# Kernel tuning notes

Measured on AMD Instinct MI355X. Metric: run time of the kernel, lower is better.

Reference implementation:

```python
import jax, jax.numpy as jnp
import numpy as np

N_NODES = 100000
EMB = 16
HID = 64
N_EDGES = 4194304


def setup_inputs() -> dict:
    key = jax.random.key(0)
    k_emb, k_e, k1, k2, k3 = jax.random.split(key, 5)
    node_embeddings = jax.random.normal(k_emb, (N_NODES, EMB), dtype=jnp.float32)
    edge_index = jax.random.randint(k_e, (2, N_EDGES), 0, N_NODES, dtype=jnp.int32)
    # MLP params: Linear(2*EMB -> HID), Linear(HID -> HID//2), Linear(HID//2 -> 1)
    s1 = 1.0 / np.sqrt(2 * EMB)
    s2 = 1.0 / np.sqrt(HID)
    s3 = 1.0 / np.sqrt(HID // 2)
    W1 = jax.random.uniform(k1, (2 * EMB, HID), jnp.float32, -s1, s1)
    b1 = jnp.zeros((HID,), jnp.float32)
    W2 = jax.random.uniform(k2, (HID, HID // 2), jnp.float32, -s2, s2)
    b2 = jnp.zeros((HID // 2,), jnp.float32)
    W3 = jax.random.uniform(k3, (HID // 2, 1), jnp.float32, -s3, s3)
    b3 = jnp.zeros((1,), jnp.float32)
    return {"node_embeddings": node_embeddings, "edge_index": edge_index,
            "W1": W1, "b1": b1, "W2": W2, "b2": b2, "W3": W3, "b3": b3}


def reference(node_embeddings, edge_index, W1, b1, W2, b2, W3, b3):
    # Gather node-pair embeddings and concat: [E, 2*EMB]
    feats = jnp.concatenate([node_embeddings[edge_index[0]],
                             node_embeddings[edge_index[1]]], axis=1)
    # 3-layer MLP (dropout is identity in eval mode)
    h = jax.nn.relu(feats @ W1 + b1)
    h = jax.nn.relu(h @ W2 + b2)
    edge_probs = jax.nn.sigmoid(h @ W3 + b3)  # [E, 1]
    return edge_probs, edge_index
```

## Files before the change

### kernel.cpp

```cpp
#include <hip/hip_runtime.h>
#include <hip/hip_bf16.h>

#define NEMB 16

typedef short s16x8 __attribute__((ext_vector_type(8)));
typedef float f32x16 __attribute__((ext_vector_type(16)));

__device__ __forceinline__ unsigned int pack_bf16x2_rnd(float lo, float hi) {
    unsigned int ul = __float_as_uint(lo);
    unsigned int uh = __float_as_uint(hi);
    return ((ul + 0x8000u) >> 16) | ((uh + 0x8000u) & 0xffff0000u);
}
__device__ __forceinline__ unsigned int pack_bf16x2_trunc(float lo, float hi) {
    return __builtin_amdgcn_perm(__float_as_uint(hi), __float_as_uint(lo),
                                 0x07060302u);
}

__global__ __launch_bounds__(256) void emb_to_bf16_kernel(
        const float* __restrict__ emb, unsigned int* __restrict__ embT,
        int nWords) {
    int i = (blockIdx.x * 256 + threadIdx.x) * 4;
    if (i + 4 <= nWords) {
        float4 a = *reinterpret_cast<const float4*>(emb + 2 * i);
        float4 b = *reinterpret_cast<const float4*>(emb + 2 * i + 4);
        uint4 r;
        r.x = pack_bf16x2_rnd(a.x, a.y);
        r.y = pack_bf16x2_rnd(a.z, a.w);
        r.z = pack_bf16x2_rnd(b.x, b.y);
        r.w = pack_bf16x2_rnd(b.z, b.w);
        *reinterpret_cast<uint4*>(embT + i) = r;
    } else {
        for (; i < nWords; ++i)
            embT[i] = pack_bf16x2_rnd(emb[2 * i], emb[2 * i + 1]);
    }
}

#define WAVES 4
#define ITERS 8
#define EDGES_PER_BLOCK (WAVES * 32 * ITERS)

__global__ __launch_bounds__(256) void edge_fused3_kernel(
        const unsigned short* __restrict__ embT,
        const int* __restrict__ ei,
        const float* __restrict__ W1, const float* __restrict__ b1,
        const float* __restrict__ W2, const float* __restrict__ b2,
        const float* __restrict__ W3, const float* __restrict__ b3,
        float* __restrict__ out, int nE) {
    const int tid = threadIdx.x;
    const int w  = tid >> 6;
    const int l  = tid & 63;
    const int el = l & 31;
    const int hi = l >> 5;

    s16x8 A1[2][2];
#pragma unroll
    for (int jt = 0; jt < 2; ++jt)
#pragma unroll
        for (int kh = 0; kh < 2; ++kh) {
            s16x8 a;
#pragma unroll
            for (int i = 0; i < 8; ++i) {
                float v = W1[(kh * 16 + hi * 8 + i) * 64 + jt * 32 + el];
                a[i] = (short)((__float_as_uint(v) + 0x8000u) >> 16);
            }
            A1[jt][kh] = a;
        }
    s16x8 A2[4];
#pragma unroll
    for (int f = 0; f < 4; ++f) {
        s16x8 a;
#pragma unroll
        for (int i = 0; i < 8; ++i) {
            float v = W2[(f * 16 + hi * 8 + i) * 32 + el];
            a[i] = (short)((__float_as_uint(v) + 0x8000u) >> 16);
        }
        A2[f] = a;
    }
    f32x16 b1v0, b1v1, b2v;
    float w3v[16];
#pragma unroll
    for (int r = 0; r < 16; ++r) {
        int n = (r & 3) + 8 * (r >> 2) + 4 * hi;
        b1v0[r] = b1[n];
        b1v1[r] = b1[32 + n];
        b2v[r]  = b2[n];
        w3v[r]  = W3[n];
    }
    const float b3v = b3[0];

    const int base0 = blockIdx.x * EDGES_PER_BLOCK + w * 32;

    int sv[ITERS], dv[ITERS];
#pragma unroll
    for (int i = 0; i < ITERS; ++i) {
        int e  = base0 + i * (WAVES * 32) + el;
        int ec = e < nE ? e : (nE - 1);
        sv[i] = ei[ec];
        dv[i] = ei[nE + ec];
    }

    auto GATHER = [&](int s, int d, uint4& es, uint4& ed) {
        es = *reinterpret_cast<const uint4*>(embT + ((size_t)s << 4) + (hi << 3));
        ed = *reinterpret_cast<const uint4*>(embT + ((size_t)d << 4) + (hi << 3));
    };

    auto COMPUTE = [&](uint4 esq, uint4 edq, int it, int s, int d) {
        union { uint4 q; s16x8 v; } es, edr;
        es.q = esq; edr.q = edq;

        f32x16 a0 = __builtin_amdgcn_mfma_f32_32x32x16_bf16(A1[0][0], es.v,  b1v0, 0, 0, 0);
        a0        = __builtin_amdgcn_mfma_f32_32x32x16_bf16(A1[0][1], edr.v, a0,   0, 0, 0);
        f32x16 a1 = __builtin_amdgcn_mfma_f32_32x32x16_bf16(A1[1][0], es.v,  b1v1, 0, 0, 0);
        a1        = __builtin_amdgcn_mfma_f32_32x32x16_bf16(A1[1][1], edr.v, a1,   0, 0, 0);

        union { unsigned int u[4]; s16x8 v; } bf0, bf1, bf2, bf3;
        {
#define MAKE_FRAG(BF, AT, M)                                                   \
            {                                                                  \
                unsigned int x0 = pack_bf16x2_trunc(fmaxf((AT)[8*(M)+0], 0.f), \
                                                    fmaxf((AT)[8*(M)+1], 0.f));\
                unsigned int x1 = pack_bf16x2_trunc(fmaxf((AT)[8*(M)+2], 0.f), \
                                                    fmaxf((AT)[8*(M)+3], 0.f));\
                unsigned int y0 = pack_bf16x2_trunc(fmaxf((AT)[8*(M)+4], 0.f), \
                                                    fmaxf((AT)[8*(M)+5], 0.f));\
                unsigned int y1 = pack_bf16x2_trunc(fmaxf((AT)[8*(M)+6], 0.f), \
                                                    fmaxf((AT)[8*(M)+7], 0.f));\
                asm("v_permlane32_swap_b32 %0, %1" : "+v"(x0), "+v"(y0));      \
                asm("v_permlane32_swap_b32 %0, %1" : "+v"(x1), "+v"(y1));      \
                BF.u[0] = x0; BF.u[1] = x1; BF.u[2] = y0; BF.u[3] = y1;        \
            }
            MAKE_FRAG(bf0, a0, 0)
            MAKE_FRAG(bf1, a0, 1)
            MAKE_FRAG(bf2, a1, 0)
            MAKE_FRAG(bf3, a1, 1)
#undef MAKE_FRAG
        }

        f32x16 acc;
        acc = __builtin_amdgcn_mfma_f32_32x32x16_bf16(A2[0], bf0.v, b2v, 0, 0, 0);
        acc = __builtin_amdgcn_mfma_f32_32x32x16_bf16(A2[1], bf1.v, acc, 0, 0, 0);
        acc = __builtin_amdgcn_mfma_f32_32x32x16_bf16(A2[2], bf2.v, acc, 0, 0, 0);
        acc = __builtin_amdgcn_mfma_f32_32x32x16_bf16(A2[3], bf3.v, acc, 0, 0, 0);

        float pr[16];
#pragma unroll
        for (int r = 0; r < 16; ++r)
            pr[r] = fmaxf(acc[r], 0.0f) * w3v[r];
        float s8[8];
#pragma unroll
        for (int r = 0; r < 8; ++r) s8[r] = pr[2 * r] + pr[2 * r + 1];
        float s4[4];
#pragma unroll
        for (int r = 0; r < 4; ++r) s4[r] = s8[2 * r] + s8[2 * r + 1];
        float v = (s4[0] + s4[1]) + (s4[2] + s4[3]);

        {
            float va = v, vb = v;
            asm("v_permlane32_swap_b32 %0, %1" : "+v"(vb), "+v"(va));
            v = va + vb;
        }

        float p = 1.0f / (1.0f + __expf(-(v + b3v)));

        int e = base0 + it * (WAVES * 32) + el;
        if (e < nE) {
            if (hi == 0) {
                out[e] = p;
                out[nE + e] = (float)s;
            } else {
                out[(size_t)2 * nE + e] = (float)d;
            }
        }
    };

    uint4 esA, edA, esB, edB;
    GATHER(sv[0], dv[0], esA, edA);
#pragma unroll
    for (int it = 0; it < ITERS; it += 2) {
        if (it + 1 < ITERS) GATHER(sv[it + 1], dv[it + 1], esB, edB);
        COMPUTE(esA, edA, it, sv[it], dv[it]);
        if (it + 2 < ITERS) GATHER(sv[it + 2], dv[it + 2], esA, edA);
        if (it + 1 < ITERS) COMPUTE(esB, edB, it + 1, sv[it + 1], dv[it + 1]);
    }
}

__global__ __launch_bounds__(256) void edge_mlp_naive_kernel(
        const float* __restrict__ emb, const int* __restrict__ ei,
        const float* __restrict__ W1, const float* __restrict__ b1,
        const float* __restrict__ W2, const float* __restrict__ b2,
        const float* __restrict__ W3, const float* __restrict__ b3,
        float* __restrict__ out, int nE) {
    __shared__ __align__(16) float sW1[32 * 64];
    __shared__ __align__(16) float sW2[64 * 32];
    __shared__ float sW3[32];
    __shared__ float sB1[64];
    __shared__ float sB2[32];
    __shared__ float sB3;
    for (int i = threadIdx.x; i < 2048; i += 256) {
        sW1[i] = W1[i];
        sW2[i] = W2[i];
    }
    if (threadIdx.x < 64) sB1[threadIdx.x] = b1[threadIdx.x];
    if (threadIdx.x < 32) {
        sW3[threadIdx.x] = W3[threadIdx.x];
        sB2[threadIdx.x] = b2[threadIdx.x];
    }
    if (threadIdx.x == 0) sB3 = b3[0];
    __syncthreads();

    int e = blockIdx.x * 256 + threadIdx.x;
    if (e >= nE) return;

    int s = ei[e];
    int d = ei[nE + e];

    float f[32];
    const float4* ps = reinterpret_cast<const float4*>(emb + (size_t)s * NEMB);
    const float4* pd = reinterpret_cast<const float4*>(emb + (size_t)d * NEMB);
#pragma unroll
    for (int q = 0; q < 4; ++q) {
        float4 v = ps[q];
        f[4 * q + 0] = v.x; f[4 * q + 1] = v.y; f[4 * q + 2] = v.z; f[4 * q + 3] = v.w;
    }
#pragma unroll
    for (int q = 0; q < 4; ++q) {
        float4 v = pd[q];
        f[16 + 4 * q + 0] = v.x; f[16 + 4 * q + 1] = v.y;
        f[16 + 4 * q + 2] = v.z; f[16 + 4 * q + 3] = v.w;
    }

    float h1[64];
#pragma unroll
    for (int j = 0; j < 64; j += 4) {
        float a0 = sB1[j + 0], a1 = sB1[j + 1], a2 = sB1[j + 2], a3 = sB1[j + 3];
#pragma unroll
        for (int k = 0; k < 32; ++k) {
            float4 wv = *reinterpret_cast<const float4*>(sW1 + k * 64 + j);
            a0 = fmaf(f[k], wv.x, a0);
            a1 = fmaf(f[k], wv.y, a1);
            a2 = fmaf(f[k], wv.z, a2);
            a3 = fmaf(f[k], wv.w, a3);
        }
        h1[j + 0] = fmaxf(a0, 0.0f);
        h1[j + 1] = fmaxf(a1, 0.0f);
        h1[j + 2] = fmaxf(a2, 0.0f);
        h1[j + 3] = fmaxf(a3, 0.0f);
    }

    float acc = sB3;
#pragma unroll
    for (int j = 0; j < 32; j += 4) {
        float a0 = sB2[j + 0], a1 = sB2[j + 1], a2 = sB2[j + 2], a3 = sB2[j + 3];
#pragma unroll
        for (int k = 0; k < 64; ++k) {
            float4 wv = *reinterpret_cast<const float4*>(sW2 + k * 32 + j);
            a0 = fmaf(h1[k], wv.x, a0);
            a1 = fmaf(h1[k], wv.y, a1);
            a2 = fmaf(h1[k], wv.z, a2);
            a3 = fmaf(h1[k], wv.w, a3);
        }
        acc = fmaf(fmaxf(a0, 0.0f), sW3[j + 0], acc);
        acc = fmaf(fmaxf(a1, 0.0f), sW3[j + 1], acc);
        acc = fmaf(fmaxf(a2, 0.0f), sW3[j + 2], acc);
        acc = fmaf(fmaxf(a3, 0.0f), sW3[j + 3], acc);
    }

    out[e] = 1.0f / (1.0f + __expf(-acc));
}

__global__ __launch_bounds__(256) void edge_idx_copy_kernel(
        const int* __restrict__ ei, float* __restrict__ out, int n) {
    int i = (blockIdx.x * 256 + threadIdx.x) * 4;
    if (i + 4 <= n) {
        int4 a = *reinterpret_cast<const int4*>(ei + i);
        float4 r = make_float4((float)a.x, (float)a.y, (float)a.z, (float)a.w);
        *reinterpret_cast<float4*>(out + i) = r;
    } else {
        for (; i < n; ++i) out[i] = (float)ei[i];
    }
}

extern "C" void kernel_launch(void* const* d_in, const int* in_sizes, int n_in,
                              void* d_out, int out_size, void* d_ws, size_t ws_size,
                              hipStream_t stream) {
    const float* emb = (const float*)d_in[0];
    const int*   ei  = (const int*)d_in[1];
    const float* W1  = (const float*)d_in[2];
    const float* b1  = (const float*)d_in[3];
    const float* W2  = (const float*)d_in[4];
    const float* b2  = (const float*)d_in[5];
    const float* W3  = (const float*)d_in[6];
    const float* b3  = (const float*)d_in[7];

    const int nNodes = in_sizes[0] / NEMB;
    const int n2E    = in_sizes[1];
    const int nE     = n2E / 2;

    float* out = (float*)d_out;

    const size_t tbl_bytes = (size_t)nNodes * NEMB * sizeof(unsigned short);
    const bool use_ws = (ws_size >= tbl_bytes);

    if (use_ws) {
        unsigned int* embT = (unsigned int*)d_ws;
        const int nWords = nNodes * 8;
        emb_to_bf16_kernel<<<(nWords / 4 + 255) / 256, 256, 0, stream>>>(
            emb, embT, nWords);

        edge_fused3_kernel<<<(nE + EDGES_PER_BLOCK - 1) / EDGES_PER_BLOCK, 256, 0,
                             stream>>>(
            (const unsigned short*)embT, ei, W1, b1, W2, b2, W3, b3, out, nE);
    } else {
        edge_mlp_naive_kernel<<<(nE + 255) / 256, 256, 0, stream>>>(
            emb, ei, W1, b1, W2, b2, W3, b3, out, nE);
        edge_idx_copy_kernel<<<((n2E + 3) / 4 + 255) / 256, 256, 0, stream>>>(
            ei, out + nE, n2E);
    }
}
```

Measured before the change: 87.15 us.

## Split edge MLP into unguarded persistent-loop kernel plus guarded tail kernel

Each block now processes 32 tiles instead of 8 in a rolled software-pipelined loop. Edge indices and embedding gathers are prefetched one to two tiles ahead, and there are no bounds checks. The per-block weight fragment setup is amortized over four times as many edges, and the grid shrinks accordingly. Any remainder edges go to a separate guarded kernel. Costs are fewer blocks in flight to hide gather latency, and an extra kernel launch when a tail exists (none for the test size).

Result: slower. 95.90 us (+10.0%).

```diff
diff --git a/kernel.cpp b/kernel.cpp
--- a/kernel.cpp
+++ b/kernel.cpp
@@ -36,10 +36,114 @@
 }
 
 #define WAVES 4
-#define ITERS 8
-#define EDGES_PER_BLOCK (WAVES * 32 * ITERS)
-
-__global__ __launch_bounds__(256) void edge_fused3_kernel(
+#define ITERS_FLAT 32
+#define EPB_FLAT (WAVES * 32 * ITERS_FLAT)
+#define ITERS_G 8
+#define EPB_G (WAVES * 32 * ITERS_G)
+
+struct MlpConsts {
+    s16x8 A1[2][2];
+    s16x8 A2[4];
+    f32x16 b1v0, b1v1, b2v;
+    float w3v[16];
+    float b3v;
+};
+
+__device__ __forceinline__ void load_consts(
+        MlpConsts& C, int el, int hi,
+        const float* __restrict__ W1, const float* __restrict__ b1,
+        const float* __restrict__ W2, const float* __restrict__ b2,
+        const float* __restrict__ W3, const float* __restrict__ b3) {
+#pragma unroll
+    for (int jt = 0; jt < 2; ++jt)
+#pragma unroll
+        for (int kh = 0; kh < 2; ++kh) {
+            s16x8 a;
+#pragma unroll
+            for (int i = 0; i < 8; ++i) {
+                float v = W1[(kh * 16 + hi * 8 + i) * 64 + jt * 32 + el];
+                a[i] = (short)((__float_as_uint(v) + 0x8000u) >> 16);
+            }
+            C.A1[jt][kh] = a;
+        }
+#pragma unroll
+    for (int f = 0; f < 4; ++f) {
+        s16x8 a;
+#pragma unroll
+        for (int i = 0; i < 8; ++i) {
+            float v = W2[(f * 16 + hi * 8 + i) * 32 + el];
+            a[i] = (short)((__float_as_uint(v) + 0x8000u) >> 16);
+        }
+        C.A2[f] = a;
+    }
+#pragma unroll
+    for (int r = 0; r < 16; ++r) {
+        int n = (r & 3) + 8 * (r >> 2) + 4 * hi;
+        C.b1v0[r] = b1[n];
+        C.b1v1[r] = b1[32 + n];
+        C.b2v[r]  = b2[n];
+        C.w3v[r]  = W3[n];
+    }
+    C.b3v = b3[0];
+}
+
+__device__ __forceinline__ float tile_mlp(const MlpConsts& C,
+                                          uint4 esq, uint4 edq) {
+    union { uint4 q; s16x8 v; } es, edr;
+    es.q = esq; edr.q = edq;
+
+    f32x16 a0 = __builtin_amdgcn_mfma_f32_32x32x16_bf16(C.A1[0][0], es.v,  C.b1v0, 0, 0, 0);
+    a0        = __builtin_amdgcn_mfma_f32_32x32x16_bf16(C.A1[0][1], edr.v, a0,     0, 0, 0);
+    f32x16 a1 = __builtin_amdgcn_mfma_f32_32x32x16_bf16(C.A1[1][0], es.v,  C.b1v1, 0, 0, 0);
+    a1        = __builtin_amdgcn_mfma_f32_32x32x16_bf16(C.A1[1][1], edr.v, a1,     0, 0, 0);
+
+    union { unsigned int u[4]; s16x8 v; } bf0, bf1, bf2, bf3;
+#define MAKE_FRAG(BF, AT, M)                                                   \
+    {                                                                          \
+        unsigned int x0 = pack_bf16x2_trunc(fmaxf((AT)[8*(M)+0], 0.f),         \
+                                            fmaxf((AT)[8*(M)+1], 0.f));        \
+        unsigned int x1 = pack_bf16x2_trunc(fmaxf((AT)[8*(M)+2], 0.f),         \
+                                            fmaxf((AT)[8*(M)+3], 0.f));        \
+        unsigned int y0 = pack_bf16x2_trunc(fmaxf((AT)[8*(M)+4], 0.f),         \
+                                            fmaxf((AT)[8*(M)+5], 0.f));        \
+        unsigned int y1 = pack_bf16x2_trunc(fmaxf((AT)[8*(M)+6], 0.f),         \
+                                            fmaxf((AT)[8*(M)+7], 0.f));        \
+        asm("v_permlane32_swap_b32 %0, %1" : "+v"(x0), "+v"(y0));              \
+        asm("v_permlane32_swap_b32 %0, %1" : "+v"(x1), "+v"(y1));              \
+        BF.u[0] = x0; BF.u[1] = x1; BF.u[2] = y0; BF.u[3] = y1;                \
+    }
+    MAKE_FRAG(bf0, a0, 0)
+    MAKE_FRAG(bf1, a0, 1)
+    MAKE_FRAG(bf2, a1, 0)
+    MAKE_FRAG(bf3, a1, 1)
+#undef MAKE_FRAG
+
+    f32x16 acc;
+    acc = __builtin_amdgcn_mfma_f32_32x32x16_bf16(C.A2[0], bf0.v, C.b2v, 0, 0, 0);
+    acc = __builtin_amdgcn_mfma_f32_32x32x16_bf16(C.A2[1], bf1.v, acc,   0, 0, 0);
+    acc = __builtin_amdgcn_mfma_f32_32x32x16_bf16(C.A2[2], bf2.v, acc,   0, 0, 0);
+    acc = __builtin_amdgcn_mfma_f32_32x32x16_bf16(C.A2[3], bf3.v, acc,   0, 0, 0);
+
+    float pr[16];
+#pragma unroll
+    for (int r = 0; r < 16; ++r)
+        pr[r] = fmaxf(acc[r], 0.0f) * C.w3v[r];
+    float s8[8];
+#pragma unroll
+    for (int r = 0; r < 8; ++r) s8[r] = pr[2 * r] + pr[2 * r + 1];
+    float s4[4];
+#pragma unroll
+    for (int r = 0; r < 4; ++r) s4[r] = s8[2 * r] + s8[2 * r + 1];
+    float v = (s4[0] + s4[1]) + (s4[2] + s4[3]);
+    {
+        float va = v, vb = v;
+        asm("v_permlane32_swap_b32 %0, %1" : "+v"(vb), "+v"(va));
+        v = va + vb;
+    }
+    return 1.0f / (1.0f + __expf(-(v + C.b3v)));
+}
+
+__global__ __launch_bounds__(256) void edge_flat_kernel(
         const unsigned short* __restrict__ embT,
         const int* __restrict__ ei,
         const float* __restrict__ W1, const float* __restrict__ b1,
@@ -52,47 +156,78 @@
     const int el = l & 31;
     const int hi = l >> 5;
 
-    s16x8 A1[2][2];
-#pragma unroll
-    for (int jt = 0; jt < 2; ++jt)
-#pragma unroll
-        for (int kh = 0; kh < 2; ++kh) {
-            s16x8 a;
-#pragma unroll
-            for (int i = 0; i < 8; ++i) {
-                float v = W1[(kh * 16 + hi * 8 + i) * 64 + jt * 32 + el];
-                a[i] = (short)((__float_as_uint(v) + 0x8000u) >> 16);
-            }
-            A1[jt][kh] = a;
-        }
-    s16x8 A2[4];
-#pragma unroll
-    for (int f = 0; f < 4; ++f) {
-        s16x8 a;
-#pragma unroll
-        for (int i = 0; i < 8; ++i) {
-            float v = W2[(f * 16 + hi * 8 + i) * 32 + el];
-            a[i] = (short)((__float_as_uint(v) + 0x8000u) >> 16);
-        }
-        A2[f] = a;
-    }
-    f32x16 b1v0, b1v1, b2v;
-    float w3v[16];
-#pragma unroll
-    for (int r = 0; r < 16; ++r) {
-        int n = (r & 3) + 8 * (r >> 2) + 4 * hi;
-        b1v0[r] = b1[n];
-        b1v1[r] = b1[32 + n];
-        b2v[r]  = b2[n];
-        w3v[r]  = W3[n];
-    }
-    const float b3v = b3[0];
-
-    const int base0 = blockIdx.x * EDGES_PER_BLOCK + w * 32;
-
-    int sv[ITERS], dv[ITERS];
-#pragma unroll
-    for (int i = 0; i < ITERS; ++i) {
+    MlpConsts C;
+    load_consts(C, el, hi, W1, b1, W2, b2, W3, b3);
+
+    const int e0 = blockIdx.x * EPB_FLAT + w * 32 + el;
+
+    auto GATHER = [&](int s, int d, uint4& es, uint4& ed) {
+        es = *reinterpret_cast<const uint4*>(embT + ((size_t)s << 4) + (hi << 3));
+        ed = *reinterpret_cast<const uint4*>(embT + ((size_t)d << 4) + (hi << 3));
+    };
+    auto STORE = [&](float p, int e, int s, int d) {
+        if (hi == 0) {
+            out[e] = p;
+            out[nE + e] = (float)s;
+        } else {
+            out[(size_t)2 * nE + e] = (float)d;
+        }
+    };
+
+    int sA = ei[e0];
+    int dA = ei[nE + e0];
+    uint4 esA, edA, esB, edB;
+    GATHER(sA, dA, esA, edA);
+    int sB = ei[e0 + 128];
+    int dB = ei[nE + e0 + 128];
+
+#pragma unroll 1
+    for (int it = 0; it < ITERS_FLAT; it += 2) {
+        GATHER(sB, dB, esB, edB);
+        int sN = 0, dN = 0;
+        if (it + 2 < ITERS_FLAT) {
+            sN = ei[e0 + (it + 2) * 128];
+            dN = ei[nE + e0 + (it + 2) * 128];
+        }
+        {
+            float p = tile_mlp(C, esA, edA);
+            STORE(p, e0 + it * 128, sA, dA);
+        }
+        if (it + 2 < ITERS_FLAT) GATHER(sN, dN, esA, edA);
+        int sM = 0, dM = 0;
+        if (it + 3 < ITERS_FLAT) {
+            sM = ei[e0 + (it + 3) * 128];
+            dM = ei[nE + e0 + (it + 3) * 128];
+        }
+        {
+            float p = tile_mlp(C, esB, edB);
+            STORE(p, e0 + (it + 1) * 128, sB, dB);
+        }
+        sA = sN; dA = dN; sB = sM; dB = dM;
+    }
+}
+
+__global__ __launch_bounds__(256) void edge_guard_kernel(
+        const unsigned short* __restrict__ embT,
+        const int* __restrict__ ei,
+        const float* __restrict__ W1, const float* __restrict__ b1,
+        const float* __restrict__ W2, const float* __restrict__ b2,
+        const float* __restrict__ W3, const float* __restrict__ b3,
+        float* __restrict__ out, int nE, int eStart) {
+    const int tid = threadIdx.x;
+    const int w  = tid >> 6;
+    const int l  = tid & 63;
+    const int el = l & 31;
+    const int hi = l >> 5;
+
+    MlpConsts C;
+    load_consts(C, el, hi, W1, b1, W2, b2, W3, b3);
+
+    const int base0 = eStart + blockIdx.x * EPB_G + w * 32;
+
+    int sv[ITERS_G], dv[ITERS_G];
+#pragma unroll
+    for (int i = 0; i < ITERS_G; ++i) {
         int e  = base0 + i * (WAVES * 32) + el;
         int ec = e < nE ? e : (nE - 1);
         sv[i] = ei[ec];
@@ -103,65 +238,8 @@
         es = *reinterpret_cast<const uint4*>(embT + ((size_t)s << 4) + (hi << 3));
         ed = *reinterpret_cast<const uint4*>(embT + ((size_t)d << 4) + (hi << 3));
     };
-
-    auto COMPUTE = [&](uint4 esq, uint4 edq, int it, int s, int d) {
-        union { uint4 q; s16x8 v; } es, edr;
-        es.q = esq; edr.q = edq;
-
-        f32x16 a0 = __builtin_amdgcn_mfma_f32_32x32x16_bf16(A1[0][0], es.v,  b1v0, 0, 0, 0);
-        a0        = __builtin_amdgcn_mfma_f32_32x32x16_bf16(A1[0][1], edr.v, a0,   0, 0, 0);
-        f32x16 a1 = __builtin_amdgcn_mfma_f32_32x32x16_bf16(A1[1][0], es.v,  b1v1, 0, 0, 0);
-        a1        = __builtin_amdgcn_mfma_f32_32x32x16_bf16(A1[1][1], edr.v, a1,   0, 0, 0);
-
-        union { unsigned int u[4]; s16x8 v; } bf0, bf1, bf2, bf3;
-        {
-#define MAKE_FRAG(BF, AT, M)                                                   \
-            {                                                                  \
-                unsigned int x0 = pack_bf16x2_trunc(fmaxf((AT)[8*(M)+0], 0.f), \
-                                                    fmaxf((AT)[8*(M)+1], 0.f));\
-                unsigned int x1 = pack_bf16x2_trunc(fmaxf((AT)[8*(M)+2], 0.f), \
-                                                    fmaxf((AT)[8*(M)+3], 0.f));\
-                unsigned int y0 = pack_bf16x2_trunc(fmaxf((AT)[8*(M)+4], 0.f), \
-                                                    fmaxf((AT)[8*(M)+5], 0.f));\
-                unsigned int y1 = pack_bf16x2_trunc(fmaxf((AT)[8*(M)+6], 0.f), \
-                                                    fmaxf((AT)[8*(M)+7], 0.f));\
-                asm("v_permlane32_swap_b32 %0, %1" : "+v"(x0), "+v"(y0));      \
-                asm("v_permlane32_swap_b32 %0, %1" : "+v"(x1), "+v"(y1));      \
-                BF.u[0] = x0; BF.u[1] = x1; BF.u[2] = y0; BF.u[3] = y1;        \
-            }
-            MAKE_FRAG(bf0, a0, 0)
-            MAKE_FRAG(bf1, a0, 1)
-            MAKE_FRAG(bf2, a1, 0)
-            MAKE_FRAG(bf3, a1, 1)
-#undef MAKE_FRAG
-        }
-
-        f32x16 acc;
-        acc = __builtin_amdgcn_mfma_f32_32x32x16_bf16(A2[0], bf0.v, b2v, 0, 0, 0);
-        acc = __builtin_amdgcn_mfma_f32_32x32x16_bf16(A2[1], bf1.v, acc, 0, 0, 0);
-        acc = __builtin_amdgcn_mfma_f32_32x32x16_bf16(A2[2], bf2.v, acc, 0, 0, 0);
-        acc = __builtin_amdgcn_mfma_f32_32x32x16_bf16(A2[3], bf3.v, acc, 0, 0, 0);
-
-        float pr[16];
-#pragma unroll
-        for (int r = 0; r < 16; ++r)
-            pr[r] = fmaxf(acc[r], 0.0f) * w3v[r];
-        float s8[8];
-#pragma unroll
-        for (int r = 0; r < 8; ++r) s8[r] = pr[2 * r] + pr[2 * r + 1];
-        float s4[4];
-#pragma unroll
-        for (int r = 0; r < 4; ++r) s4[r] = s8[2 * r] + s8[2 * r + 1];
-        float v = (s4[0] + s4[1]) + (s4[2] + s4[3]);
-
-        {
-            float va = v, vb = v;
-            asm("v_permlane32_swap_b32 %0, %1" : "+v"(vb), "+v"(va));
-            v = va + vb;
-        }
-
-        float p = 1.0f / (1.0f + __expf(-(v + b3v)));
-
+    auto DO_TILE = [&](uint4 es, uint4 ed, int it, int s, int d) {
+        float p = tile_mlp(C, es, ed);
         int e = base0 + it * (WAVES * 32) + el;
         if (e < nE) {
             if (hi == 0) {
@@ -176,11 +254,12 @@
     uint4 esA, edA, esB, edB;
     GATHER(sv[0], dv[0], esA, edA);
 #pragma unroll
-    for (int it = 0; it < ITERS; it += 2) {
-        if (it + 1 < ITERS) GATHER(sv[it + 1], dv[it + 1], esB, edB);
-        COMPUTE(esA, edA, it, sv[it], dv[it]);
-        if (it + 2 < ITERS) GATHER(sv[it + 2], dv[it + 2], esA, edA);
-        if (it + 1 < ITERS) COMPUTE(esB, edB, it + 1, sv[it + 1], dv[it + 1]);
+    for (int it = 0; it < ITERS_G; it += 2) {
+        if (base0 + it * (WAVES * 32) >= nE) break;
+        if (it + 1 < ITERS_G) GATHER(sv[it + 1], dv[it + 1], esB, edB);
+        DO_TILE(esA, edA, it, sv[it], dv[it]);
+        if (it + 2 < ITERS_G) GATHER(sv[it + 2], dv[it + 2], esA, edA);
+        if (it + 1 < ITERS_G) DO_TILE(esB, edB, it + 1, sv[it + 1], dv[it + 1]);
     }
 }
 
@@ -307,9 +386,19 @@
         emb_to_bf16_kernel<<<(nWords / 4 + 255) / 256, 256, 0, stream>>>(
             emb, embT, nWords);
 
-        edge_fused3_kernel<<<(nE + EDGES_PER_BLOCK - 1) / EDGES_PER_BLOCK, 256, 0,
-                             stream>>>(
-            (const unsigned short*)embT, ei, W1, b1, W2, b2, W3, b3, out, nE);
+        const int nFlatBlocks = nE / EPB_FLAT;
+        const int nFlat = nFlatBlocks * EPB_FLAT;
+        if (nFlatBlocks > 0) {
+            edge_flat_kernel<<<nFlatBlocks, 256, 0, stream>>>(
+                (const unsigned short*)embT, ei, W1, b1, W2, b2, W3, b3, out, nE);
+        }
+        const int rem = nE - nFlat;
+        if (rem > 0) {
+            const int gBlocks = (rem + EPB_G - 1) / EPB_G;
+            edge_guard_kernel<<<gBlocks, 256, 0, stream>>>(
+                (const unsigned short*)embT, ei, W1, b1, W2, b2, W3, b3, out, nE,
+                nFlat);
+        }
     } else {
         edge_mlp_naive_kernel<<<(nE + 255) / 256, 256, 0, stream>>>(
             emb, ei, W1, b1, W2, b2, W3, b3, out, nE);
```

## Deepen gather prefetch to two tiles ahead and raise wave priority around MFMA

Applied to the files above, without the earlier changes.

Replaces the two-buffer gather/compute loop with a three-buffer rotation, so each embedding gather is issued two tiles before its compute instead of one. This is meant to hide more of the random-access gather latency behind MFMA work. It also wraps the MFMA section in s_setprio(1)/s_setprio(0) to favour waves issuing matrix work. The extra in-flight buffers raise VGPR use and could lower occupancy.

Result: no change. 87.75 us (+0.7%).

```diff
diff --git a/kernel.cpp b/kernel.cpp
--- a/kernel.cpp
+++ b/kernel.cpp
@@ -39,7 +39,7 @@
 #define ITERS 8
 #define EDGES_PER_BLOCK (WAVES * 32 * ITERS)
 
-__global__ __launch_bounds__(256) void edge_fused3_kernel(
+__global__ __launch_bounds__(256) void edge_fused4_kernel(
         const unsigned short* __restrict__ embT,
         const int* __restrict__ ei,
         const float* __restrict__ W1, const float* __restrict__ b1,
@@ -104,43 +104,43 @@
         ed = *reinterpret_cast<const uint4*>(embT + ((size_t)d << 4) + (hi << 3));
     };
 
-    auto COMPUTE = [&](uint4 esq, uint4 edq, int it, int s, int d) {
+    auto DO_TILE = [&](uint4 esq, uint4 edq, int it, int s, int d) {
         union { uint4 q; s16x8 v; } es, edr;
         es.q = esq; edr.q = edq;
 
+        __builtin_amdgcn_s_setprio(1);
         f32x16 a0 = __builtin_amdgcn_mfma_f32_32x32x16_bf16(A1[0][0], es.v,  b1v0, 0, 0, 0);
         a0        = __builtin_amdgcn_mfma_f32_32x32x16_bf16(A1[0][1], edr.v, a0,   0, 0, 0);
         f32x16 a1 = __builtin_amdgcn_mfma_f32_32x32x16_bf16(A1[1][0], es.v,  b1v1, 0, 0, 0);
         a1        = __builtin_amdgcn_mfma_f32_32x32x16_bf16(A1[1][1], edr.v, a1,   0, 0, 0);
 
         union { unsigned int u[4]; s16x8 v; } bf0, bf1, bf2, bf3;
-        {
 #define MAKE_FRAG(BF, AT, M)                                                   \
-            {                                                                  \
-                unsigned int x0 = pack_bf16x2_trunc(fmaxf((AT)[8*(M)+0], 0.f), \
-                                                    fmaxf((AT)[8*(M)+1], 0.f));\
-                unsigned int x1 = pack_bf16x2_trunc(fmaxf((AT)[8*(M)+2], 0.f), \
-                                                    fmaxf((AT)[8*(M)+3], 0.f));\
-                unsigned int y0 = pack_bf16x2_trunc(fmaxf((AT)[8*(M)+4], 0.f), \
-                                                    fmaxf((AT)[8*(M)+5], 0.f));\
-                unsigned int y1 = pack_bf16x2_trunc(fmaxf((AT)[8*(M)+6], 0.f), \
-                                                    fmaxf((AT)[8*(M)+7], 0.f));\
-                asm("v_permlane32_swap_b32 %0, %1" : "+v"(x0), "+v"(y0));      \
-                asm("v_permlane32_swap_b32 %0, %1" : "+v"(x1), "+v"(y1));      \
-                BF.u[0] = x0; BF.u[1] = x1; BF.u[2] = y0; BF.u[3] = y1;        \
-            }
-            MAKE_FRAG(bf0, a0, 0)
-            MAKE_FRAG(bf1, a0, 1)
-            MAKE_FRAG(bf2, a1, 0)
-            MAKE_FRAG(bf3, a1, 1)
+        {                                                                      \
+            unsigned int x0 = pack_bf16x2_trunc(fmaxf((AT)[8*(M)+0], 0.f),     \
+                                                fmaxf((AT)[8*(M)+1], 0.f));    \
+            unsigned int x1 = pack_bf16x2_trunc(fmaxf((AT)[8*(M)+2], 0.f),     \
+                                                fmaxf((AT)[8*(M)+3], 0.f));    \
+            unsigned int y0 = pack_bf16x2_trunc(fmaxf((AT)[8*(M)+4], 0.f),     \
+                                                fmaxf((AT)[8*(M)+5], 0.f));    \
+            unsigned int y1 = pack_bf16x2_trunc(fmaxf((AT)[8*(M)+6], 0.f),     \
+                                                fmaxf((AT)[8*(M)+7], 0.f));    \
+            asm("v_permlane32_swap_b32 %0, %1" : "+v"(x0), "+v"(y0));          \
+            asm("v_permlane32_swap_b32 %0, %1" : "+v"(x1), "+v"(y1));          \
+            BF.u[0] = x0; BF.u[1] = x1; BF.u[2] = y0; BF.u[3] = y1;            \
+        }
+        MAKE_FRAG(bf0, a0, 0)
+        MAKE_FRAG(bf1, a0, 1)
+        MAKE_FRAG(bf2, a1, 0)
+        MAKE_FRAG(bf3, a1, 1)
 #undef MAKE_FRAG
-        }
 
         f32x16 acc;
         acc = __builtin_amdgcn_mfma_f32_32x32x16_bf16(A2[0], bf0.v, b2v, 0, 0, 0);
         acc = __builtin_amdgcn_mfma_f32_32x32x16_bf16(A2[1], bf1.v, acc, 0, 0, 0);
         acc = __builtin_amdgcn_mfma_f32_32x32x16_bf16(A2[2], bf2.v, acc, 0, 0, 0);
         acc = __builtin_amdgcn_mfma_f32_32x32x16_bf16(A2[3], bf3.v, acc, 0, 0, 0);
+        __builtin_amdgcn_s_setprio(0);
 
         float pr[16];
 #pragma unroll
@@ -153,7 +153,6 @@
 #pragma unroll
         for (int r = 0; r < 4; ++r) s4[r] = s8[2 * r] + s8[2 * r + 1];
         float v = (s4[0] + s4[1]) + (s4[2] + s4[3]);
-
         {
             float va = v, vb = v;
             asm("v_permlane32_swap_b32 %0, %1" : "+v"(vb), "+v"(va));
@@ -173,15 +172,18 @@
         }
     };
 
-    uint4 esA, edA, esB, edB;
-    GATHER(sv[0], dv[0], esA, edA);
-#pragma unroll
-    for (int it = 0; it < ITERS; it += 2) {
-        if (it + 1 < ITERS) GATHER(sv[it + 1], dv[it + 1], esB, edB);
-        COMPUTE(esA, edA, it, sv[it], dv[it]);
-        if (it + 2 < ITERS) GATHER(sv[it + 2], dv[it + 2], esA, edA);
-        if (it + 1 < ITERS) COMPUTE(esB, edB, it + 1, sv[it + 1], dv[it + 1]);
-    }
+    uint4 esX, edX, esY, edY, esZ, edZ;
+    GATHER(sv[0], dv[0], esX, edX);
+    GATHER(sv[1], dv[1], esY, edY);
+
+    GATHER(sv[2], dv[2], esZ, edZ);  DO_TILE(esX, edX, 0, sv[0], dv[0]);
+    GATHER(sv[3], dv[3], esX, edX);  DO_TILE(esY, edY, 1, sv[1], dv[1]);
+    GATHER(sv[4], dv[4], esY, edY);  DO_TILE(esZ, edZ, 2, sv[2], dv[2]);
+    GATHER(sv[5], dv[5], esZ, edZ);  DO_TILE(esX, edX, 3, sv[3], dv[3]);
+    GATHER(sv[6], dv[6], esX, edX);  DO_TILE(esY, edY, 4, sv[4], dv[4]);
+    GATHER(sv[7], dv[7], esY, edY);  DO_TILE(esZ, edZ, 5, sv[5], dv[5]);
+    DO_TILE(esX, edX, 6, sv[6], dv[6]);
+    DO_TILE(esY, edY, 7, sv[7], dv[7]);
 }
 
 __global__ __launch_bounds__(256) void edge_mlp_naive_kernel(
@@ -307,7 +309,7 @@
         emb_to_bf16_kernel<<<(nWords / 4 + 255) / 256, 256, 0, stream>>>(
             emb, embT, nWords);
 
-        edge_fused3_kernel<<<(nE + EDGES_PER_BLOCK - 1) / EDGES_PER_BLOCK, 256, 0,
+        edge_fused4_kernel<<<(nE + EDGES_PER_BLOCK - 1) / EDGES_PER_BLOCK, 256, 0,
                              stream>>>(
             (const unsigned short*)embT, ei, W1, b1, W2, b2, W3, b3, out, nE);
     } else {
```
